# Optimization experiments

Hardware: AMD Instinct MI355X
Metric: run time of the kernel (lower is better)

Reference implementation:

```python
import jax, jax.numpy as jnp
import numpy as np

B, S, H2 = 32, 4096, 512  # H2 = 2*hidden_size


def setup_inputs() -> dict:
    key = jax.random.key(0)
    ks = jax.random.split(key, 10)
    s = 1.0 / np.sqrt(H2)
    return {
        "decoder_state": jax.random.normal(ks[0], (B, 1, H2), jnp.float32),
        "encoder_outputs": jax.random.normal(ks[1], (B, S, H2), jnp.float32),
        "coverage_vector": jax.random.uniform(ks[2], (B, S, H2), jnp.float32),
        "W_h": jax.random.uniform(ks[3], (H2, H2), jnp.float32, -s, s),
        "b_h": jax.random.uniform(ks[4], (H2,), jnp.float32, -s, s),
        "W_s": jax.random.uniform(ks[5], (H2, H2), jnp.float32, -s, s),
        "b_s": jax.random.uniform(ks[6], (H2,), jnp.float32, -s, s),
        "W_c": jax.random.uniform(ks[7], (H2, H2), jnp.float32, -s, s),
        "b_c": jax.random.uniform(ks[8], (H2,), jnp.float32, -s, s),
        "v": jax.random.uniform(ks[9], (H2, 1), jnp.float32, -s, s),
    }


def reference(decoder_state, encoder_outputs, coverage_vector,
              W_h, b_h, W_s, b_s, W_c, b_c, v):
    # additive attention features: [B, S, 2H]
    e = jnp.tanh(encoder_outputs @ W_h + b_h
                 + decoder_state @ W_s + b_s      # broadcasts over S
                 + coverage_vector @ W_c + b_c)
    scores = e @ v                                # [B, S, 1]
    attn_dist = jax.nn.softmax(scores, axis=1)    # softmax over source positions
    # weighted sum of encoder outputs: [B, 1, 2H]
    h_star_t = jnp.einsum('bsi,bsd->bid', attn_dist, encoder_outputs)
    coverage_new = coverage_vector + attn_dist    # broadcast over feature dim
    return h_star_t, attn_dist, coverage_new
```

## Files before the change

kernel.cpp:

```cpp
#include <hip/hip_runtime.h>
#include <hip/hip_bf16.h>
#include <stdint.h>

#define H2    512
#define BATCH 32
#define SEQ   4096
#define BM    64
#define BK    64
#define NKT   16

typedef __attribute__((ext_vector_type(4))) float f32x4;
typedef __attribute__((ext_vector_type(8))) short bf16x8;

__device__ __forceinline__ unsigned short f2bf(float f) {
    union { float f; unsigned u; } v; v.f = f;
    unsigned r = v.u + 0x7FFF + ((v.u >> 16) & 1);
    return (unsigned short)(r >> 16);
}

__device__ __forceinline__ float fast_tanh(float x) {
    float e = __builtin_amdgcn_exp2f(x * 2.88539008177793f);
    return 1.0f - 2.0f * __builtin_amdgcn_rcpf(e + 1.0f);
}

__global__ void kprep_w(const float* __restrict__ Wh, const float* __restrict__ Wc,
                        unsigned short* __restrict__ wt) {
    int c    = blockIdx.x * blockDim.x + threadIdx.x;
    int lane = c & 63;
    int cb   = (c >> 6) & 31;
    int ks   = (c >> 11) & 1;
    int kt   = c >> 12;
    int col  = cb * 16 + (lane & 15);
    int k0   = kt * 64 + ks * 32 + (lane >> 4) * 8;
    unsigned short tmp[8];
#pragma unroll
    for (int j = 0; j < 8; ++j) {
        int kg = k0 + j;
        float w = (kg < 512) ? Wh[kg * 512 + col] : Wc[(kg - 512) * 512 + col];
        tmp[j] = f2bf(w);
    }
    *reinterpret_cast<uint4*>(wt + (size_t)c * 8) = *reinterpret_cast<const uint4*>(tmp);
}

__global__ void kprep_q(const float* __restrict__ dec, const float* __restrict__ Ws,
                        const float* __restrict__ bh, const float* __restrict__ bs,
                        const float* __restrict__ bc, float* __restrict__ q) {
    __shared__ float dsh[512];
    int b = blockIdx.x, t = threadIdx.x;
    dsh[t]       = dec[b * 512 + t];
    dsh[t + 256] = dec[b * 512 + 256 + t];
    __syncthreads();
    float a0 = 0.f, a1 = 0.f;
#pragma unroll 4
    for (int k = 0; k < 512; ++k) {
        float d = dsh[k];
        a0 = fmaf(d, Ws[k * 512 + t], a0);
        a1 = fmaf(d, Ws[k * 512 + 256 + t], a1);
    }
    q[b * 512 + t]       = a0 + bh[t] + bs[t] + bc[t];
    q[b * 512 + 256 + t] = a1 + bh[256 + t] + bs[256 + t] + bc[256 + t];
}

__launch_bounds__(512, 4)
__global__ void kgemm(const float* __restrict__ enc, const float* __restrict__ cov,
                      const unsigned short* __restrict__ wt,
                      const float* __restrict__ q, const float* __restrict__ vvec,
                      float* __restrict__ scores) {
    __shared__ unsigned short Asm[2][BM * BK];
    __shared__ float qv[H2];
    __shared__ float vv[H2];
    __shared__ float sred[BM][8];

    int tid  = threadIdx.x;
    int lane = tid & 63, wn = tid >> 6;

    int cpx  = gridDim.x >> 3;
    int swz  = (blockIdx.x & 7) * cpx + (blockIdx.x >> 3);
    int row0 = swz * BM;

    qv[tid] = q[(row0 >> 12) * H2 + tid];
    vv[tid] = vvec[tid];

    int r = tid >> 3, k8 = tid & 7;
    const float* ae = enc + (size_t)(row0 + r) * H2 + k8 * 8;
    const float* ac = cov + (size_t)(row0 + r) * H2 + k8 * 8;
    unsigned awb = (unsigned)(r * 128 + ((k8 * 16) ^ ((r & 7) << 4)));

    unsigned arb0 = (unsigned)((lane & 15) * 128 +
                    ((((lane >> 4) << 4))      ^ ((lane & 7) << 4)));
    unsigned arb1 = (unsigned)((lane & 15) * 128 +
                    (((64 + ((lane >> 4) << 4))) ^ ((lane & 7) << 4)));

    f32x4 acc[4][4] = {};

    {
        f32x4 a0 = *reinterpret_cast<const f32x4*>(ae);
        f32x4 a1 = *reinterpret_cast<const f32x4*>(ae + 4);
        union { unsigned short h[8]; uint4 u; } t;
#pragma unroll
        for (int j = 0; j < 4; ++j) { t.h[j] = f2bf(a0[j]); t.h[4 + j] = f2bf(a1[j]); }
        *reinterpret_cast<uint4*>((char*)Asm[0] + awb) = t.u;
    }
    __syncthreads();

    for (int kt = 0; kt < NKT; ++kt) {
        int cur = kt & 1;
        bf16x8 bfr[2][4];
        const bf16x8* bp0 = reinterpret_cast<const bf16x8*>(wt) +
                            ((size_t)(kt * 2 + 0) * 32 + wn * 4) * 64 + lane;
        const bf16x8* bp1 = reinterpret_cast<const bf16x8*>(wt) +
                            ((size_t)(kt * 2 + 1) * 32 + wn * 4) * 64 + lane;
#pragma unroll
        for (int ni = 0; ni < 4; ++ni) bfr[0][ni] = bp0[ni * 64];
#pragma unroll
        for (int ni = 0; ni < 4; ++ni) bfr[1][ni] = bp1[ni * 64];
        f32x4 p0, p1;
        if (kt + 1 < NKT) {
            const float* src = (kt + 1 < 8) ? (ae + (kt + 1) * 64) : (ac + (kt - 7) * 64);
            p0 = *reinterpret_cast<const f32x4*>(src);
            p1 = *reinterpret_cast<const f32x4*>(src + 4);
        }
#pragma unroll
        for (int ks = 0; ks < 2; ++ks) {
            bf16x8 af[4];
#pragma unroll
            for (int mi = 0; mi < 4; ++mi)
                af[mi] = *reinterpret_cast<const bf16x8*>(
                    (const char*)Asm[cur] + mi * 2048 + (ks ? arb1 : arb0));
#pragma unroll
            for (int mi = 0; mi < 4; ++mi)
#pragma unroll
                for (int ni = 0; ni < 4; ++ni)
                    acc[mi][ni] = __builtin_amdgcn_mfma_f32_16x16x32_bf16(
                        af[mi], bfr[ks][ni], acc[mi][ni], 0, 0, 0);
        }
        if (kt + 1 < NKT) {
            union { unsigned short h[8]; uint4 u; } t;
#pragma unroll
            for (int j = 0; j < 4; ++j) { t.h[j] = f2bf(p0[j]); t.h[4 + j] = f2bf(p1[j]); }
            *reinterpret_cast<uint4*>((char*)Asm[cur ^ 1] + awb) = t.u;
        }
        __syncthreads();
    }

    float ps[4][4] = {};
#pragma unroll
    for (int mi = 0; mi < 4; ++mi)
#pragma unroll
        for (int ni = 0; ni < 4; ++ni) {
            int colg = wn * 64 + ni * 16 + (lane & 15);
            float qq = qv[colg], vl = vv[colg];
#pragma unroll
            for (int j = 0; j < 4; ++j) {
                float e = fast_tanh(acc[mi][ni][j] + qq);
                ps[mi][j] = fmaf(e, vl, ps[mi][j]);
            }
        }
#pragma unroll
    for (int mi = 0; mi < 4; ++mi)
#pragma unroll
        for (int j = 0; j < 4; ++j) {
            float s = ps[mi][j];
            s += __shfl_xor(s, 1);
            s += __shfl_xor(s, 2);
            s += __shfl_xor(s, 4);
            s += __shfl_xor(s, 8);
            if ((lane & 15) == 0)
                sred[mi * 16 + (lane >> 4) * 4 + j][wn] = s;
        }
    __syncthreads();
    if (tid < BM) {
        float s = 0.f;
#pragma unroll
        for (int w = 0; w < 8; ++w) s += sred[tid][w];
        scores[row0 + tid] = s;
    }
}

__global__ void ksoftmax(const float* __restrict__ scores, float* __restrict__ out) {
    __shared__ float redm[16];
    __shared__ float reds[16];
    int b = blockIdx.x, t = threadIdx.x, lane = t & 63, w = t >> 6;
    if (t < 512) out[b * 512 + t] = 0.0f;
    f32x4 sv = *reinterpret_cast<const f32x4*>(scores + b * 4096 + t * 4);
    float m = fmaxf(fmaxf(sv[0], sv[1]), fmaxf(sv[2], sv[3]));
#pragma unroll
    for (int o = 1; o < 64; o <<= 1) m = fmaxf(m, __shfl_xor(m, o));
    if (lane == 0) redm[w] = m;
    __syncthreads();
    float mm = redm[0];
#pragma unroll
    for (int i = 1; i < 16; ++i) mm = fmaxf(mm, redm[i]);

    f32x4 p;
#pragma unroll
    for (int j = 0; j < 4; ++j)
        p[j] = __builtin_amdgcn_exp2f((sv[j] - mm) * 1.4426950408889634f);
    float s = p[0] + p[1] + p[2] + p[3];
#pragma unroll
    for (int o = 1; o < 64; o <<= 1) s += __shfl_xor(s, o);
    if (lane == 0) reds[w] = s;
    __syncthreads();
    float tot = 0.f;
#pragma unroll
    for (int i = 0; i < 16; ++i) tot += reds[i];
    float rinv = __builtin_amdgcn_rcpf(tot);
    p *= rinv;
    *reinterpret_cast<f32x4*>(out + 16384 + b * 4096 + t * 4) = p;
}

__global__ void kcov(const float* __restrict__ enc, const float* __restrict__ cov,
                     float* __restrict__ out) {
    const float* attn = out + 16384;
    float* covn  = out + 16384 + 131072;
    float* hstar = out;
    int blk = blockIdx.x;
    int b = blk >> 6, ck = blk & 63;
    int s0 = ck * 64;
    int t  = threadIdx.x;
    int f4 = (t & 127) * 4;
    int rp = t >> 7;
    size_t base = (size_t)b * SEQ * H2;
    f32x4 h = {0.f, 0.f, 0.f, 0.f};
#pragma unroll 2
    for (int i = 0; i < 32; ++i) {
        int s = s0 + i * 2 + rp;
        float a = attn[b * 4096 + s];
        size_t idx = base + (size_t)s * H2 + f4;
        f32x4 e4 = *reinterpret_cast<const f32x4*>(enc + idx);
        f32x4 c4 = *reinterpret_cast<const f32x4*>(cov + idx);
        c4 += a;
        __builtin_nontemporal_store(c4, reinterpret_cast<f32x4*>(covn + idx));
        h += a * e4;
    }
    int off = b * 512 + f4;
    atomicAdd(&hstar[off + 0], h[0]);
    atomicAdd(&hstar[off + 1], h[1]);
    atomicAdd(&hstar[off + 2], h[2]);
    atomicAdd(&hstar[off + 3], h[3]);
}

extern "C" void kernel_launch(void* const* d_in, const int* in_sizes, int n_in,
                              void* d_out, int out_size, void* d_ws, size_t ws_size,
                              hipStream_t stream) {
    const float* dec = (const float*)d_in[0];
    const float* enc = (const float*)d_in[1];
    const float* cov = (const float*)d_in[2];
    const float* Wh  = (const float*)d_in[3];
    const float* bh  = (const float*)d_in[4];
    const float* Ws  = (const float*)d_in[5];
    const float* bs  = (const float*)d_in[6];
    const float* Wc  = (const float*)d_in[7];
    const float* bc  = (const float*)d_in[8];
    const float* v   = (const float*)d_in[9];
    float* out = (float*)d_out;

    char* ws = (char*)d_ws;
    unsigned short* wt = (unsigned short*)ws;
    float* q      = (float*)(ws + (1 << 20));
    float* scores = (float*)(ws + (1 << 20) + 65536);

    kprep_w <<<dim3(256),  dim3(256),  0, stream>>>(Wh, Wc, wt);
    kprep_q <<<dim3(32),   dim3(256),  0, stream>>>(dec, Ws, bh, bs, bc, q);
    kgemm   <<<dim3(2048), dim3(512),  0, stream>>>(enc, cov, wt, q, v, scores);
    ksoftmax<<<dim3(32),   dim3(1024), 0, stream>>>(scores, out);
    kcov    <<<dim3(2048), dim3(256),  0, stream>>>(enc, cov, out);
}
```

Baseline: 401.5 us.

## Deepen GEMM prefetch pipeline with register double-buffered weights and two-ahead A loads

Restructures the kgemm main loop so that weight fragments for the next k-tile and the fp32 A tile two steps ahead are loaded into register double buffers while the current tile's MFMAs run. All LDS A-fragments are read up front, MFMAs are raised in priority with s_setprio, and __syncthreads is replaced by an explicit lgkmcnt wait plus s_barrier fenced with sched_barriers. Launch bounds drop to 2 waves-per-EU minimum, which allows more registers for the extra buffers but may lower occupancy for this memory-bound kernel.

```diff
diff --git a/kernel.cpp b/kernel.cpp
--- a/kernel.cpp
+++ b/kernel.cpp
@@ -61,7 +61,7 @@
     q[b * 512 + 256 + t] = a1 + bh[256 + t] + bs[256 + t] + bc[256 + t];
 }
 
-__launch_bounds__(512, 4)
+__launch_bounds__(512, 2)
 __global__ void kgemm(const float* __restrict__ enc, const float* __restrict__ cov,
                       const unsigned short* __restrict__ wt,
                       const float* __restrict__ q, const float* __restrict__ vvec,
@@ -86,61 +86,84 @@
     const float* ac = cov + (size_t)(row0 + r) * H2 + k8 * 8;
     unsigned awb = (unsigned)(r * 128 + ((k8 * 16) ^ ((r & 7) << 4)));
 
-    unsigned arb0 = (unsigned)((lane & 15) * 128 +
-                    ((((lane >> 4) << 4))      ^ ((lane & 7) << 4)));
-    unsigned arb1 = (unsigned)((lane & 15) * 128 +
-                    (((64 + ((lane >> 4) << 4))) ^ ((lane & 7) << 4)));
-
-    f32x4 acc[4][4] = {};
-
+    unsigned arb[2];
+    arb[0] = (unsigned)((lane & 15) * 128 +
+             ((((lane >> 4) << 4))        ^ ((lane & 7) << 4)));
+    arb[1] = (unsigned)((lane & 15) * 128 +
+             (((64 + ((lane >> 4) << 4))) ^ ((lane & 7) << 4)));
+
+    const bf16x8* bb = reinterpret_cast<const bf16x8*>(wt) + (size_t)wn * 4 * 64 + lane;
+
+    f32x4  acc[4][4] = {};
+    bf16x8 bfr[2][2][4];
+    f32x4  pA[2][2];
+
+#pragma unroll
+    for (int ks = 0; ks < 2; ++ks)
+#pragma unroll
+        for (int ni = 0; ni < 4; ++ni)
+            bfr[0][ks][ni] = bb[ks * 2048 + ni * 64];
     {
         f32x4 a0 = *reinterpret_cast<const f32x4*>(ae);
         f32x4 a1 = *reinterpret_cast<const f32x4*>(ae + 4);
+        pA[0][0] = *reinterpret_cast<const f32x4*>(ae + 64);
+        pA[0][1] = *reinterpret_cast<const f32x4*>(ae + 68);
         union { unsigned short h[8]; uint4 u; } t;
 #pragma unroll
         for (int j = 0; j < 4; ++j) { t.h[j] = f2bf(a0[j]); t.h[4 + j] = f2bf(a1[j]); }
         *reinterpret_cast<uint4*>((char*)Asm[0] + awb) = t.u;
     }
-    __syncthreads();
-
+    asm volatile("s_waitcnt lgkmcnt(0)" ::: "memory");
+    __builtin_amdgcn_sched_barrier(0);
+    __builtin_amdgcn_s_barrier();
+    __builtin_amdgcn_sched_barrier(0);
+
+#pragma unroll
     for (int kt = 0; kt < NKT; ++kt) {
-        int cur = kt & 1;
-        bf16x8 bfr[2][4];
-        const bf16x8* bp0 = reinterpret_cast<const bf16x8*>(wt) +
-                            ((size_t)(kt * 2 + 0) * 32 + wn * 4) * 64 + lane;
-        const bf16x8* bp1 = reinterpret_cast<const bf16x8*>(wt) +
-                            ((size_t)(kt * 2 + 1) * 32 + wn * 4) * 64 + lane;
-#pragma unroll
-        for (int ni = 0; ni < 4; ++ni) bfr[0][ni] = bp0[ni * 64];
-#pragma unroll
-        for (int ni = 0; ni < 4; ++ni) bfr[1][ni] = bp1[ni * 64];
-        f32x4 p0, p1;
+        const int cur = kt & 1, nxt = cur ^ 1;
+        bf16x8 af[2][4];
+#pragma unroll
+        for (int ks = 0; ks < 2; ++ks)
+#pragma unroll
+            for (int mi = 0; mi < 4; ++mi)
+                af[ks][mi] = *reinterpret_cast<const bf16x8*>(
+                    (const char*)Asm[cur] + mi * 2048 + arb[ks]);
         if (kt + 1 < NKT) {
-            const float* src = (kt + 1 < 8) ? (ae + (kt + 1) * 64) : (ac + (kt - 7) * 64);
-            p0 = *reinterpret_cast<const f32x4*>(src);
-            p1 = *reinterpret_cast<const f32x4*>(src + 4);
-        }
-#pragma unroll
-        for (int ks = 0; ks < 2; ++ks) {
-            bf16x8 af[4];
-#pragma unroll
-            for (int mi = 0; mi < 4; ++mi)
-                af[mi] = *reinterpret_cast<const bf16x8*>(
-                    (const char*)Asm[cur] + mi * 2048 + (ks ? arb1 : arb0));
+#pragma unroll
+            for (int ks = 0; ks < 2; ++ks)
+#pragma unroll
+                for (int ni = 0; ni < 4; ++ni)
+                    bfr[nxt][ks][ni] = bb[(size_t)((kt + 1) * 2 + ks) * 2048 + ni * 64];
+        }
+        if (kt + 2 < NKT) {
+            const float* src = (kt + 2 < 8) ? (ae + (kt + 2) * 64) : (ac + (kt - 6) * 64);
+            pA[nxt][0] = *reinterpret_cast<const f32x4*>(src);
+            pA[nxt][1] = *reinterpret_cast<const f32x4*>(src + 4);
+        }
+        __builtin_amdgcn_sched_barrier(0);
+        __builtin_amdgcn_s_setprio(1);
+#pragma unroll
+        for (int ks = 0; ks < 2; ++ks)
 #pragma unroll
             for (int mi = 0; mi < 4; ++mi)
 #pragma unroll
                 for (int ni = 0; ni < 4; ++ni)
                     acc[mi][ni] = __builtin_amdgcn_mfma_f32_16x16x32_bf16(
-                        af[mi], bfr[ks][ni], acc[mi][ni], 0, 0, 0);
-        }
+                        af[ks][mi], bfr[cur][ks][ni], acc[mi][ni], 0, 0, 0);
+        __builtin_amdgcn_s_setprio(0);
         if (kt + 1 < NKT) {
             union { unsigned short h[8]; uint4 u; } t;
 #pragma unroll
-            for (int j = 0; j < 4; ++j) { t.h[j] = f2bf(p0[j]); t.h[4 + j] = f2bf(p1[j]); }
-            *reinterpret_cast<uint4*>((char*)Asm[cur ^ 1] + awb) = t.u;
-        }
-        __syncthreads();
+            for (int j = 0; j < 4; ++j) {
+                t.h[j]     = f2bf(pA[cur][0][j]);
+                t.h[4 + j] = f2bf(pA[cur][1][j]);
+            }
+            *reinterpret_cast<uint4*>((char*)Asm[nxt] + awb) = t.u;
+        }
+        asm volatile("s_waitcnt lgkmcnt(0)" ::: "memory");
+        __builtin_amdgcn_sched_barrier(0);
+        __builtin_amdgcn_s_barrier();
+        __builtin_amdgcn_sched_barrier(0);
     }
 
     float ps[4][4] = {};
```

Result: slower. 411.8 us (+2.6%).

## Stage weight tiles in LDS via async global_load_lds with a K=32 double-buffered pipeline

Applied to the files above, without the earlier changes.

The GEMM kernel stops loading bf16 weight fragments straight from global memory into registers. It now streams them into double-buffered LDS with asynchronous global_load_lds, halves the K step to 32, and loads the A tile with only half the threads. Explicit waitcnt and barriers plus raised MFMA priority are meant to overlap memory traffic with compute. The cost is 72KB of dynamic LDS per block, which limits occupancy to about two 512-thread blocks per CU, and twice as many barriers per tile.

```diff
diff --git a/kernel.cpp b/kernel.cpp
--- a/kernel.cpp
+++ b/kernel.cpp
@@ -6,11 +6,14 @@
 #define BATCH 32
 #define SEQ   4096
 #define BM    64
-#define BK    64
-#define NKT   16
+#define BKS   32
+#define NKT3  32
 
 typedef __attribute__((ext_vector_type(4))) float f32x4;
 typedef __attribute__((ext_vector_type(8))) short bf16x8;
+
+typedef __attribute__((address_space(3))) unsigned int       as3_uint;
+typedef const __attribute__((address_space(1))) unsigned int as1_uint;
 
 __device__ __forceinline__ unsigned short f2bf(float f) {
     union { float f; unsigned u; } v; v.f = f;
@@ -28,10 +31,9 @@
     int c    = blockIdx.x * blockDim.x + threadIdx.x;
     int lane = c & 63;
     int cb   = (c >> 6) & 31;
-    int ks   = (c >> 11) & 1;
-    int kt   = c >> 12;
+    int kt   = c >> 11;
     int col  = cb * 16 + (lane & 15);
-    int k0   = kt * 64 + ks * 32 + (lane >> 4) * 8;
+    int k0   = kt * 32 + (lane >> 4) * 8;
     unsigned short tmp[8];
 #pragma unroll
     for (int j = 0; j < 8; ++j) {
@@ -66,10 +68,9 @@
                       const unsigned short* __restrict__ wt,
                       const float* __restrict__ q, const float* __restrict__ vvec,
                       float* __restrict__ scores) {
-    __shared__ unsigned short Asm[2][BM * BK];
-    __shared__ float qv[H2];
-    __shared__ float vv[H2];
-    __shared__ float sred[BM][8];
+    extern __shared__ char lds[];
+    unsigned short* Bsm = (unsigned short*)lds;
+    unsigned short* Asm = (unsigned short*)(lds + 65536);
 
     int tid  = threadIdx.x;
     int lane = tid & 63, wn = tid >> 6;
@@ -78,70 +79,95 @@
     int swz  = (blockIdx.x & 7) * cpx + (blockIdx.x >> 3);
     int row0 = swz * BM;
 
+    int r = tid >> 2, k8 = tid & 3;
+    const float* aeb = enc + (size_t)(row0 + r) * H2 + k8 * 8;
+    const float* acb = cov + (size_t)(row0 + r) * H2 + k8 * 8;
+    unsigned awb = (unsigned)((r >> 4) * 1024 + k8 * 256 +
+                              (((r & 15) * 16) ^ (k8 << 4)));
+    unsigned arb = (unsigned)((lane >> 4) * 256 +
+                              (((lane & 15) * 16) ^ ((lane >> 4) << 4)));
+    unsigned brb = (unsigned)(wn * 4096 + lane * 16);
+    const unsigned short* gsrc = wt + ((size_t)wn * 4 * 64 + lane) * 8;
+
+    f32x4 acc[4][4] = {};
+    f32x4 pA0, pA1;
+
+    if (tid < 256) {
+        pA0 = *reinterpret_cast<const f32x4*>(aeb);
+        pA1 = *reinterpret_cast<const f32x4*>(aeb + 4);
+    }
+#pragma unroll
+    for (int i = 0; i < 4; ++i)
+        __builtin_amdgcn_global_load_lds(
+            (as1_uint*)(gsrc + (size_t)i * 512),
+            (as3_uint*)((char*)Bsm + wn * 4096 + i * 1024), 16, 0, 0);
+    if (tid < 256) {
+        union { unsigned short h[8]; uint4 u; } u;
+#pragma unroll
+        for (int j = 0; j < 4; ++j) { u.h[j] = f2bf(pA0[j]); u.h[4 + j] = f2bf(pA1[j]); }
+        *reinterpret_cast<uint4*>((char*)Asm + awb) = u.u;
+    }
+    asm volatile("s_waitcnt lgkmcnt(0)" ::: "memory");
+    __builtin_amdgcn_sched_barrier(0);
+    __builtin_amdgcn_s_barrier();
+    __builtin_amdgcn_sched_barrier(0);
+
+#pragma unroll 2
+    for (int t = 0; t < NKT3; ++t) {
+        const int cur = t & 1, nxt = cur ^ 1;
+        asm volatile("s_waitcnt vmcnt(0)" ::: "memory");
+        __builtin_amdgcn_sched_barrier(0);
+        if (t + 1 < NKT3 && tid < 256) {
+            const float* src = (t + 1 < 16) ? (aeb + (t + 1) * 32)
+                                            : (acb + (t - 15) * 32);
+            pA0 = *reinterpret_cast<const f32x4*>(src);
+            pA1 = *reinterpret_cast<const f32x4*>(src + 4);
+        }
+        bf16x8 af[4], bf[4];
+#pragma unroll
+        for (int mi = 0; mi < 4; ++mi)
+            af[mi] = *reinterpret_cast<const bf16x8*>(
+                (char*)Asm + cur * 4096 + mi * 1024 + arb);
+#pragma unroll
+        for (int ni = 0; ni < 4; ++ni)
+            bf[ni] = *reinterpret_cast<const bf16x8*>(
+                (char*)Bsm + cur * 32768 + ni * 1024 + brb);
+        if (t + 1 < NKT3) {
+            const unsigned short* gs = gsrc + (size_t)(t + 1) * 32 * 64 * 8;
+#pragma unroll
+            for (int i = 0; i < 4; ++i)
+                __builtin_amdgcn_global_load_lds(
+                    (as1_uint*)(gs + (size_t)i * 512),
+                    (as3_uint*)((char*)Bsm + nxt * 32768 + wn * 4096 + i * 1024),
+                    16, 0, 0);
+        }
+        __builtin_amdgcn_sched_barrier(0);
+        __builtin_amdgcn_s_setprio(1);
+#pragma unroll
+        for (int mi = 0; mi < 4; ++mi)
+#pragma unroll
+            for (int ni = 0; ni < 4; ++ni)
+                acc[mi][ni] = __builtin_amdgcn_mfma_f32_16x16x32_bf16(
+                    af[mi], bf[ni], acc[mi][ni], 0, 0, 0);
+        __builtin_amdgcn_s_setprio(0);
+        if (t + 1 < NKT3 && tid < 256) {
+            union { unsigned short h[8]; uint4 u; } u;
+#pragma unroll
+            for (int j = 0; j < 4; ++j) { u.h[j] = f2bf(pA0[j]); u.h[4 + j] = f2bf(pA1[j]); }
+            *reinterpret_cast<uint4*>((char*)Asm + nxt * 4096 + awb) = u.u;
+        }
+        asm volatile("s_waitcnt lgkmcnt(0)" ::: "memory");
+        __builtin_amdgcn_sched_barrier(0);
+        __builtin_amdgcn_s_barrier();
+        __builtin_amdgcn_sched_barrier(0);
+    }
+
+    float* qv   = (float*)lds;
+    float* vv   = qv + 512;
+    float* sred = vv + 512;
     qv[tid] = q[(row0 >> 12) * H2 + tid];
     vv[tid] = vvec[tid];
-
-    int r = tid >> 3, k8 = tid & 7;
-    const float* ae = enc + (size_t)(row0 + r) * H2 + k8 * 8;
-    const float* ac = cov + (size_t)(row0 + r) * H2 + k8 * 8;
-    unsigned awb = (unsigned)(r * 128 + ((k8 * 16) ^ ((r & 7) << 4)));
-
-    unsigned arb0 = (unsigned)((lane & 15) * 128 +
-                    ((((lane >> 4) << 4))      ^ ((lane & 7) << 4)));
-    unsigned arb1 = (unsigned)((lane & 15) * 128 +
-                    (((64 + ((lane >> 4) << 4))) ^ ((lane & 7) << 4)));
-
-    f32x4 acc[4][4] = {};
-
-    {
-        f32x4 a0 = *reinterpret_cast<const f32x4*>(ae);
-        f32x4 a1 = *reinterpret_cast<const f32x4*>(ae + 4);
-        union { unsigned short h[8]; uint4 u; } t;
-#pragma unroll
-        for (int j = 0; j < 4; ++j) { t.h[j] = f2bf(a0[j]); t.h[4 + j] = f2bf(a1[j]); }
-        *reinterpret_cast<uint4*>((char*)Asm[0] + awb) = t.u;
-    }
-    __syncthreads();
-
-    for (int kt = 0; kt < NKT; ++kt) {
-        int cur = kt & 1;
-        bf16x8 bfr[2][4];
-        const bf16x8* bp0 = reinterpret_cast<const bf16x8*>(wt) +
-                            ((size_t)(kt * 2 + 0) * 32 + wn * 4) * 64 + lane;
-        const bf16x8* bp1 = reinterpret_cast<const bf16x8*>(wt) +
-                            ((size_t)(kt * 2 + 1) * 32 + wn * 4) * 64 + lane;
-#pragma unroll
-        for (int ni = 0; ni < 4; ++ni) bfr[0][ni] = bp0[ni * 64];
-#pragma unroll
-        for (int ni = 0; ni < 4; ++ni) bfr[1][ni] = bp1[ni * 64];
-        f32x4 p0, p1;
-        if (kt + 1 < NKT) {
-            const float* src = (kt + 1 < 8) ? (ae + (kt + 1) * 64) : (ac + (kt - 7) * 64);
-            p0 = *reinterpret_cast<const f32x4*>(src);
-            p1 = *reinterpret_cast<const f32x4*>(src + 4);
-        }
-#pragma unroll
-        for (int ks = 0; ks < 2; ++ks) {
-            bf16x8 af[4];
-#pragma unroll
-            for (int mi = 0; mi < 4; ++mi)
-                af[mi] = *reinterpret_cast<const bf16x8*>(
-                    (const char*)Asm[cur] + mi * 2048 + (ks ? arb1 : arb0));
-#pragma unroll
-            for (int mi = 0; mi < 4; ++mi)
-#pragma unroll
-                for (int ni = 0; ni < 4; ++ni)
-                    acc[mi][ni] = __builtin_amdgcn_mfma_f32_16x16x32_bf16(
-                        af[mi], bfr[ks][ni], acc[mi][ni], 0, 0, 0);
-        }
-        if (kt + 1 < NKT) {
-            union { unsigned short h[8]; uint4 u; } t;
-#pragma unroll
-            for (int j = 0; j < 4; ++j) { t.h[j] = f2bf(p0[j]); t.h[4 + j] = f2bf(p1[j]); }
-            *reinterpret_cast<uint4*>((char*)Asm[cur ^ 1] + awb) = t.u;
-        }
-        __syncthreads();
-    }
+    __syncthreads();
 
     float ps[4][4] = {};
 #pragma unroll
@@ -166,13 +192,13 @@
             s += __shfl_xor(s, 4);
             s += __shfl_xor(s, 8);
             if ((lane & 15) == 0)
-                sred[mi * 16 + (lane >> 4) * 4 + j][wn] = s;
+                sred[(mi * 16 + (lane >> 4) * 4 + j) * 8 + wn] = s;
         }
     __syncthreads();
     if (tid < BM) {
         float s = 0.f;
 #pragma unroll
-        for (int w = 0; w < 8; ++w) s += sred[tid][w];
+        for (int w = 0; w < 8; ++w) s += sred[tid * 8 + w];
         scores[row0 + tid] = s;
     }
 }
@@ -260,9 +286,16 @@
     float* q      = (float*)(ws + (1 << 20));
     float* scores = (float*)(ws + (1 << 20) + 65536);
 
-    kprep_w <<<dim3(256),  dim3(256),  0, stream>>>(Wh, Wc, wt);
-    kprep_q <<<dim3(32),   dim3(256),  0, stream>>>(dec, Ws, bh, bs, bc, q);
-    kgemm   <<<dim3(2048), dim3(512),  0, stream>>>(enc, cov, wt, q, v, scores);
-    ksoftmax<<<dim3(32),   dim3(1024), 0, stream>>>(scores, out);
-    kcov    <<<dim3(2048), dim3(256),  0, stream>>>(enc, cov, out);
-}
+    static bool attr_done = false;
+    if (!attr_done) {
+        hipFuncSetAttribute((const void*)kgemm,
+                            hipFuncAttributeMaxDynamicSharedMemorySize, 73728);
+        attr_done = true;
+    }
+
+    kprep_w <<<dim3(256),  dim3(256),  0,     stream>>>(Wh, Wc, wt);
+    kprep_q <<<dim3(32),   dim3(256),  0,     stream>>>(dec, Ws, bh, bs, bc, q);
+    kgemm   <<<dim3(2048), dim3(512),  73728, stream>>>(enc, cov, wt, q, v, scores);
+    ksoftmax<<<dim3(32),   dim3(1024), 0,     stream>>>(scores, out);
+    kcov    <<<dim3(2048), dim3(256),  0,     stream>>>(enc, cov, out);
+}
```

Result: slower. 414.8 us (+3.3%).

## Restructure GEMM main loop with 128-wide K stages and interleaved prefetch

Applied to the files above, without the earlier changes.

Rewrites the fused encoder/coverage GEMM loop to use 128-wide K stages split into four 32-wide MFMA sub-steps. Global A loads, B fragment loads and the next stage's LDS writes are interleaved between MFMA groups using sched_barrier, raised wave priority around the MFMAs, and explicit lgkmcnt fences. The float-to-bf16 conversion now uses the hardware packed v_cvt_pk_bf16_f32 instruction instead of software rounding. The weight prep layout is reindexed to match the new per-32-K tiling. This halves the number of block barriers and aims to hide memory latency, but LDS use doubles to 32 KB, which can reduce occupancy.

```diff
diff --git a/kernel.cpp b/kernel.cpp
--- a/kernel.cpp
+++ b/kernel.cpp
@@ -6,8 +6,6 @@
 #define BATCH 32
 #define SEQ   4096
 #define BM    64
-#define BK    64
-#define NKT   16
 
 typedef __attribute__((ext_vector_type(4))) float f32x4;
 typedef __attribute__((ext_vector_type(8))) short bf16x8;
@@ -16,6 +14,13 @@
     union { float f; unsigned u; } v; v.f = f;
     unsigned r = v.u + 0x7FFF + ((v.u >> 16) & 1);
     return (unsigned short)(r >> 16);
+}
+
+__device__ __forceinline__ uint2 cvt4_bf16(f32x4 a) {
+    uint2 r;
+    asm("v_cvt_pk_bf16_f32 %0, %1, %2" : "=v"(r.x) : "v"(a[0]), "v"(a[1]));
+    asm("v_cvt_pk_bf16_f32 %0, %1, %2" : "=v"(r.y) : "v"(a[2]), "v"(a[3]));
+    return r;
 }
 
 __device__ __forceinline__ float fast_tanh(float x) {
@@ -28,10 +33,9 @@
     int c    = blockIdx.x * blockDim.x + threadIdx.x;
     int lane = c & 63;
     int cb   = (c >> 6) & 31;
-    int ks   = (c >> 11) & 1;
-    int kt   = c >> 12;
+    int kt   = c >> 11;
     int col  = cb * 16 + (lane & 15);
-    int k0   = kt * 64 + ks * 32 + (lane >> 4) * 8;
+    int k0   = kt * 32 + (lane >> 4) * 8;
     unsigned short tmp[8];
 #pragma unroll
     for (int j = 0; j < 8; ++j) {
@@ -66,7 +70,7 @@
                       const unsigned short* __restrict__ wt,
                       const float* __restrict__ q, const float* __restrict__ vvec,
                       float* __restrict__ scores) {
-    __shared__ unsigned short Asm[2][BM * BK];
+    __shared__ unsigned short Asm[2][8192];
     __shared__ float qv[H2];
     __shared__ float vv[H2];
     __shared__ float sred[BM][8];
@@ -78,70 +82,110 @@
     int swz  = (blockIdx.x & 7) * cpx + (blockIdx.x >> 3);
     int row0 = swz * BM;
 
+    int r = tid >> 3, k8 = tid & 7;
+    const float* aeb = enc + (size_t)(row0 + r) * H2;
+    const float* acb = cov + (size_t)(row0 + r) * H2;
+    unsigned awq = (unsigned)((r >> 4) * 1024 + (k8 & 3) * 256 +
+                              (((r & 15) * 16) ^ ((k8 & 3) << 4)));
+    unsigned aw0 = ((k8 >> 2) + 0) * 4096 + awq;
+    unsigned aw1 = ((k8 >> 2) + 2) * 4096 + awq;
+    unsigned arb = (unsigned)((lane >> 4) * 256 +
+                              (((lane & 15) * 16) ^ ((lane >> 4) << 4)));
+    const bf16x8* bb = reinterpret_cast<const bf16x8*>(wt) +
+                       (size_t)(wn * 4) * 64 + lane;
+
+    f32x4  acc[4][4] = {};
+    bf16x8 bfr[4];
+    bf16x8 af[4];
+    f32x4  pa0, pa1;
+
+#define DS_AF(CUR, S)                                                          \
+    _Pragma("unroll")                                                          \
+    for (int mi = 0; mi < 4; ++mi)                                             \
+        af[mi] = *reinterpret_cast<const bf16x8*>(                             \
+            (char*)Asm + (CUR) * 16384 + (S) * 4096 + mi * 1024 + arb);
+#define LOAD_B(KT)                                                             \
+    { const int _kt = (KT);                                                    \
+      _Pragma("unroll")                                                        \
+      for (int ni = 0; ni < 4; ++ni)                                           \
+          bfr[ni] = bb[(size_t)_kt * 2048 + ni * 64]; }
+#define MFMA16                                                                 \
+    __builtin_amdgcn_s_setprio(1);                                             \
+    _Pragma("unroll")                                                          \
+    for (int mi = 0; mi < 4; ++mi)                                             \
+        _Pragma("unroll")                                                      \
+        for (int ni = 0; ni < 4; ++ni)                                         \
+            acc[mi][ni] = __builtin_amdgcn_mfma_f32_16x16x32_bf16(             \
+                af[mi], bfr[ni], acc[mi][ni], 0, 0, 0);                        \
+    __builtin_amdgcn_s_setprio(0);
+#define ISSUE_A(ST1, H)                                                        \
+    { int _c = (ST1) * 128 + (H) * 64 + k8 * 8;                                \
+      const float* _p = (_c < 512) ? (aeb + _c) : (acb + (_c - 512));          \
+      pa0 = *reinterpret_cast<const f32x4*>(_p);                               \
+      pa1 = *reinterpret_cast<const f32x4*>(_p + 4); }
+#define WRITE_A(BUF, AW)                                                       \
+    { uint2 _u0 = cvt4_bf16(pa0); uint2 _u1 = cvt4_bf16(pa1);                  \
+      uint4 _u; _u.x = _u0.x; _u.y = _u0.y; _u.z = _u1.x; _u.w = _u1.y;        \
+      *reinterpret_cast<uint4*>((char*)Asm + (BUF) * 16384 + (AW)) = _u; }
+#define SB0 __builtin_amdgcn_sched_barrier(0);
+#define FENCE_BAR                                                              \
+    asm volatile("s_waitcnt lgkmcnt(0)" ::: "memory");                         \
+    SB0 __builtin_amdgcn_s_barrier(); SB0
+
+#define BODY(ST, CUR, MORE)                                                    \
+  {                                                                            \
+    const int kt0 = (ST) * 4;                                                  \
+    DS_AF(CUR, 0)                                                              \
+    MFMA16                                                                     \
+    SB0                                                                        \
+    DS_AF(CUR, 1)                                                              \
+    LOAD_B(kt0 + 1)                                                            \
+    if (MORE) { ISSUE_A((ST) + 1, 0) }                                         \
+    SB0                                                                        \
+    MFMA16                                                                     \
+    SB0                                                                        \
+    DS_AF(CUR, 2)                                                              \
+    LOAD_B(kt0 + 2)                                                            \
+    SB0                                                                        \
+    MFMA16                                                                     \
+    SB0                                                                        \
+    DS_AF(CUR, 3)                                                              \
+    LOAD_B(kt0 + 3)                                                            \
+    if (MORE) { WRITE_A((CUR) ^ 1, aw0) ISSUE_A((ST) + 1, 1) }                 \
+    SB0                                                                        \
+    MFMA16                                                                     \
+    SB0                                                                        \
+    LOAD_B((kt0 + 4 < 32) ? kt0 + 4 : 31)                                      \
+    if (MORE) { WRITE_A((CUR) ^ 1, aw1) }                                      \
+    FENCE_BAR                                                                  \
+  }
+
+    LOAD_B(0)
+    ISSUE_A(0, 0)
+    WRITE_A(0, aw0)
+    ISSUE_A(0, 1)
+    WRITE_A(0, aw1)
+    FENCE_BAR
+
+#pragma unroll 1
+    for (int stp = 0; stp < 4; ++stp) {
+        const int st0 = stp * 2;
+        BODY(st0, 0, true)
+        BODY(st0 + 1, 1, (stp < 3))
+    }
+
+#undef DS_AF
+#undef LOAD_B
+#undef MFMA16
+#undef ISSUE_A
+#undef WRITE_A
+#undef SB0
+#undef FENCE_BAR
+#undef BODY
+
     qv[tid] = q[(row0 >> 12) * H2 + tid];
     vv[tid] = vvec[tid];
-
-    int r = tid >> 3, k8 = tid & 7;
-    const float* ae = enc + (size_t)(row0 + r) * H2 + k8 * 8;
-    const float* ac = cov + (size_t)(row0 + r) * H2 + k8 * 8;
-    unsigned awb = (unsigned)(r * 128 + ((k8 * 16) ^ ((r & 7) << 4)));
-
-    unsigned arb0 = (unsigned)((lane & 15) * 128 +
-                    ((((lane >> 4) << 4))      ^ ((lane & 7) << 4)));
-    unsigned arb1 = (unsigned)((lane & 15) * 128 +
-                    (((64 + ((lane >> 4) << 4))) ^ ((lane & 7) << 4)));
-
-    f32x4 acc[4][4] = {};
-
-    {
-        f32x4 a0 = *reinterpret_cast<const f32x4*>(ae);
-        f32x4 a1 = *reinterpret_cast<const f32x4*>(ae + 4);
-        union { unsigned short h[8]; uint4 u; } t;
-#pragma unroll
-        for (int j = 0; j < 4; ++j) { t.h[j] = f2bf(a0[j]); t.h[4 + j] = f2bf(a1[j]); }
-        *reinterpret_cast<uint4*>((char*)Asm[0] + awb) = t.u;
-    }
-    __syncthreads();
-
-    for (int kt = 0; kt < NKT; ++kt) {
-        int cur = kt & 1;
-        bf16x8 bfr[2][4];
-        const bf16x8* bp0 = reinterpret_cast<const bf16x8*>(wt) +
-                            ((size_t)(kt * 2 + 0) * 32 + wn * 4) * 64 + lane;
-        const bf16x8* bp1 = reinterpret_cast<const bf16x8*>(wt) +
-                            ((size_t)(kt * 2 + 1) * 32 + wn * 4) * 64 + lane;
-#pragma unroll
-        for (int ni = 0; ni < 4; ++ni) bfr[0][ni] = bp0[ni * 64];
-#pragma unroll
-        for (int ni = 0; ni < 4; ++ni) bfr[1][ni] = bp1[ni * 64];
-        f32x4 p0, p1;
-        if (kt + 1 < NKT) {
-            const float* src = (kt + 1 < 8) ? (ae + (kt + 1) * 64) : (ac + (kt - 7) * 64);
-            p0 = *reinterpret_cast<const f32x4*>(src);
-            p1 = *reinterpret_cast<const f32x4*>(src + 4);
-        }
-#pragma unroll
-        for (int ks = 0; ks < 2; ++ks) {
-            bf16x8 af[4];
-#pragma unroll
-            for (int mi = 0; mi < 4; ++mi)
-                af[mi] = *reinterpret_cast<const bf16x8*>(
-                    (const char*)Asm[cur] + mi * 2048 + (ks ? arb1 : arb0));
-#pragma unroll
-            for (int mi = 0; mi < 4; ++mi)
-#pragma unroll
-                for (int ni = 0; ni < 4; ++ni)
-                    acc[mi][ni] = __builtin_amdgcn_mfma_f32_16x16x32_bf16(
-                        af[mi], bfr[ks][ni], acc[mi][ni], 0, 0, 0);
-        }
-        if (kt + 1 < NKT) {
-            union { unsigned short h[8]; uint4 u; } t;
-#pragma unroll
-            for (int j = 0; j < 4; ++j) { t.h[j] = f2bf(p0[j]); t.h[4 + j] = f2bf(p1[j]); }
-            *reinterpret_cast<uint4*>((char*)Asm[cur ^ 1] + awb) = t.u;
-        }
-        __syncthreads();
-    }
+    __syncthreads();
 
     float ps[4][4] = {};
 #pragma unroll
```

Measured after the change: 564.3 us. +40.6%, slower.
